# Kernel optimization log

Hardware: AMD Instinct MI355X
Metric: run time of the kernel (lower is better)

## Reference

```python
import jax, jax.numpy as jnp
import numpy as np

N = 50000      # nodes
E = 400000     # edges
G = 128        # graphs in batch
D_NODE = 64
EDGE_DIM = 72
HEADS = 4
H0, H1, H2 = 128, 128, 64
NC = 2
NEG = 0.2      # GATConv leaky_relu negative_slope default
D1 = H2 + EDGE_DIM - 1  # ffn input dim = 135


def _p(k, shape, s=0.1):
    return jax.random.normal(k, shape, dtype=jnp.float32) * s


def setup_inputs() -> dict:
    key = jax.random.key(0)
    ks = jax.random.split(key, 24)
    x = jax.random.normal(ks[0], (N, D_NODE), dtype=jnp.float32)
    edge_index = jax.random.randint(ks[1], (2, E), 0, N)
    edge_attr = jax.random.uniform(ks[2], (E, EDGE_DIM), dtype=jnp.float32)
    batch = jnp.sort(jax.random.randint(ks[3], (N,), 0, G))
    return dict(
        x=x, edge_index=edge_index, edge_attr=edge_attr, batch=batch,
        # GATConv layer 1: in=D_NODE, out=H0, heads=HEADS, concat
        W1=_p(ks[4], (D_NODE, HEADS * H0)), We1=_p(ks[5], (EDGE_DIM, HEADS * H0)),
        as1=_p(ks[6], (HEADS, H0)), ad1=_p(ks[7], (HEADS, H0)), ae1=_p(ks[8], (HEADS, H0)),
        b1=jnp.zeros((HEADS * H0,), jnp.float32),
        # GATConv layer 2: in=HEADS*H0, out=H1, heads=HEADS, concat
        W2=_p(ks[9], (HEADS * H0, HEADS * H1)), We2=_p(ks[10], (EDGE_DIM, HEADS * H1)),
        as2=_p(ks[11], (HEADS, H1)), ad2=_p(ks[12], (HEADS, H1)), ae2=_p(ks[13], (HEADS, H1)),
        b2=jnp.zeros((HEADS * H1,), jnp.float32),
        # GATConv layer 3: in=HEADS*H1, out=H2, heads=1, concat=False
        W3=_p(ks[14], (HEADS * H1, H2)), We3=_p(ks[15], (EDGE_DIM, H2)),
        as3=_p(ks[16], (1, H2)), ad3=_p(ks[17], (1, H2)), ae3=_p(ks[18], (1, H2)),
        b3=jnp.zeros((H2,), jnp.float32),
        # ffn: Linear(135 -> 67), ReLU, Linear(67 -> 2), Softmax
        Wf1=_p(ks[19], (D1, D1 // 2)), bf1=jnp.zeros((D1 // 2,), jnp.float32),
        Wf2=_p(ks[20], (D1 // 2, NC)), bf2=jnp.zeros((NC,), jnp.float32),
    )


def _seg_softmax(s, seg, n):
    # numerically-stable softmax over segments (per-destination neighborhoods)
    m = jax.ops.segment_max(s, seg, num_segments=n)
    m = jnp.where(jnp.isfinite(m), m, 0.0)
    e = jnp.exp(s - m[seg])
    z = jax.ops.segment_sum(e, seg, num_segments=n)
    return e / (z[seg] + 1e-16)


def _gat(x, src, dst, eattr, W, We, a_s, a_d, a_e, b, heads, oc, concat):
    # PyG GATConv with edge_dim: shared src/dst projection, edge feats only in attention
    n = x.shape[0]
    xs = (x @ W).reshape(n, heads, oc)            # [N,H,C]
    ee = (eattr @ We).reshape(-1, heads, oc)      # [Ea,H,C]
    alpha = (xs * a_s).sum(-1)[src] + (xs * a_d).sum(-1)[dst] + (ee * a_e).sum(-1)
    alpha = jax.nn.leaky_relu(alpha, NEG)         # [Ea,H]
    alpha = _seg_softmax(alpha, dst, n)
    out = jax.ops.segment_sum(xs[src] * alpha[:, :, None], dst, num_segments=n)
    out = out.reshape(n, heads * oc) if concat else out.mean(axis=1)
    return out + b


def reference(x, edge_index, edge_attr, batch,
              W1, We1, as1, ad1, ae1, b1,
              W2, We2, as2, ad2, ae2, b2,
              W3, We3, as3, ad3, ae3, b3,
              Wf1, bf1, Wf2, bf2):
    src, dst = edge_index[0], edge_index[1]
    n = x.shape[0]
    # --- 1-gram feature vector: scatter-add edge_attr[:, :-1] by graph of src ---
    eb = batch[src]
    og = jax.ops.segment_sum(edge_attr[:, :-1], eb, num_segments=G)   # [G, EDGE_DIM-1]
    og = og / jnp.maximum(jnp.linalg.norm(og, axis=1, keepdims=True), 1e-12)
    # --- add self loops, edge_attr fill_value='mean' (mean over incoming edges) ---
    ones_e = jnp.ones((src.shape[0],), x.dtype)
    deg = jax.ops.segment_sum(ones_e, dst, num_segments=n)
    loop_attr = jax.ops.segment_sum(edge_attr, dst, num_segments=n) / jnp.maximum(deg, 1.0)[:, None]
    nodes = jnp.arange(n)
    src_a = jnp.concatenate([src, nodes])
    dst_a = jnp.concatenate([dst, nodes])
    ea = jnp.concatenate([edge_attr, loop_attr], axis=0)
    # --- GAT stack with ReLU activations ---
    h = jax.nn.relu(_gat(x, src_a, dst_a, ea, W1, We1, as1, ad1, ae1, b1, HEADS, H0, True))
    h = jax.nn.relu(_gat(h, src_a, dst_a, ea, W2, We2, as2, ad2, ae2, b2, HEADS, H1, True))
    h = jax.nn.relu(_gat(h, src_a, dst_a, ea, W3, We3, as3, ad3, ae3, b3, 1, H2, False))
    # --- global mean pool over graphs ---
    cnt = jax.ops.segment_sum(jnp.ones((n,), x.dtype), batch, num_segments=G)
    pooled = jax.ops.segment_sum(h, batch, num_segments=G) / jnp.maximum(cnt, 1.0)[:, None]
    # --- concat + ffn (dropout p=0 in eval) + softmax ---
    z = jnp.concatenate([pooled, og], axis=1)                         # [G, 135]
    z = jax.nn.relu(z @ Wf1 + bf1)
    return jax.nn.softmax(z @ Wf2 + bf2, axis=1)
```

## Files before the change

kernel.cpp:

```cpp
#include <hip/hip_runtime.h>

#define NNODES 50000
#define NEDGES 400000
#define NEA    450000
#define NG     128
#define DEGCAP 96
#define OGW    72
#define NCH    49
#define PREPN  1128328
#define PREPB  4408
#define EDGEB  1563
#define OGB    (NG*16)

typedef unsigned short u16;
typedef unsigned int   u32;
typedef __attribute__((ext_vector_type(8))) short short8v;
typedef __attribute__((ext_vector_type(4))) float f32x4;

static inline int ceil_div(int a, int b){ return (a + b - 1)/b; }

__device__ __forceinline__ u16 f2bf(float f){
  u32 u = __builtin_bit_cast(u32, f);
  u = (u + 0x7fffu + ((u >> 16) & 1u)) >> 16;
  return (u16)u;
}
__device__ __forceinline__ float bfLO(u32 q){ return __builtin_bit_cast(float, q << 16); }
__device__ __forceinline__ float bfHI(u32 q){ return __builtin_bit_cast(float, q & 0xffff0000u); }
__device__ __forceinline__ void gload_lds16(const u16* g, u16* l){
  __builtin_amdgcn_global_load_lds((const __attribute__((address_space(1))) void*)g,
                                   (__attribute__((address_space(3))) void*)l, 16, 0, 0);
}

__global__ void k_prep_deg(const float* __restrict__ x, u16* __restrict__ xb,
                       const float* __restrict__ W1, u16* __restrict__ Wt1,
                       const float* __restrict__ W2, u16* __restrict__ Wt2,
                       const float* __restrict__ W3, u16* __restrict__ Wt3,
                       const float* __restrict__ We1, const float* __restrict__ ae1,
                       const float* __restrict__ We2, const float* __restrict__ ae2,
                       const float* __restrict__ We3, const float* __restrict__ ae3,
                       float* __restrict__ veall,
                       const int* __restrict__ src, const int* __restrict__ dst,
                       const int* __restrict__ batch,
                       int* __restrict__ deg, int* __restrict__ gb, int* __restrict__ gcnt){
  if (blockIdx.x >= PREPB){
    __shared__ int h[NG];
    int t = threadIdx.x;
    if (t < NG) h[t] = 0;
    __syncthreads();
    int e = (blockIdx.x - PREPB)*256 + t;
    if (e < NEDGES){
      atomicAdd(&deg[dst[e]], 1);
      int g = batch[src[e]];
      gb[e] = g;
      atomicAdd(&h[g], 1);
    }
    __syncthreads();
    if (t < NG && h[t]) atomicAdd(&gcnt[t], h[t]);
    return;
  }
  int i = blockIdx.x*blockDim.x + threadIdx.x;
  if (i < 800000){
    float4 v = ((const float4*)x)[i];
    ((ushort4*)xb)[i] = make_ushort4(f2bf(v.x), f2bf(v.y), f2bf(v.z), f2bf(v.w));
    return;
  }
  i -= 800000;
  if (i < 32768){
    int n = i >> 6, k = i & 63;
    Wt1[i] = f2bf(W1[(size_t)k*512 + n]);
    return;
  }
  i -= 32768;
  if (i < 262144){
    int n = i >> 9, k = i & 511;
    Wt2[i] = f2bf(W2[(size_t)k*512 + n]);
    return;
  }
  i -= 262144;
  if (i < 32768){
    int n = i >> 9, k = i & 511;
    Wt3[i] = f2bf(W3[(size_t)k*64 + n]);
    return;
  }
  i -= 32768;
  if (i < 648){
    const float* We; const float* ae; int H, C, basej, li;
    if (i < 288){ We = We1; ae = ae1; H = 4; C = 128; basej = 0; li = i; }
    else if (i < 576){ We = We2; ae = ae2; H = 4; C = 128; basej = 4; li = i - 288; }
    else { We = We3; ae = ae3; H = 1; C = 64; basej = 8; li = i - 576; }
    int k = li / H, h = li - k*H;
    const float* wrow = We + (size_t)k*H*C + (size_t)h*C;
    const float* arow = ae + (size_t)h*C;
    float s = 0.f;
    for (int c = 0; c < C; ++c) s += wrow[c]*arow[c];
    veall[k*9 + basej + h] = s;
  }
}

__global__ __launch_bounds__(1024) void k_chunksum(const int* __restrict__ deg, int* __restrict__ csum){
  __shared__ int s[1024];
  int t = threadIdx.x;
  int i = blockIdx.x*1024 + t;
  s[t] = (i < NNODES) ? deg[i]+1 : 0;
  __syncthreads();
  for (int o = 512; o > 0; o >>= 1){
    if (t < o) s[t] += s[t+o];
    __syncthreads();
  }
  if (t == 0) csum[blockIdx.x] = s[0];
}

__global__ __launch_bounds__(128) void k_scanmid(const int* __restrict__ csum, int* __restrict__ cbase,
                                                 const int* __restrict__ gcnt, int* __restrict__ goff,
                                                 int* __restrict__ gcur){
  __shared__ int sg[NG];
  int t = threadIdx.x;
  if (t < 64){
    int v0 = (t < NCH) ? csum[t] : 0;
    int v = v0;
    #pragma unroll
    for (int o = 1; o < 64; o <<= 1){
      int xsh = __shfl_up(v, o);
      if (t >= o) v += xsh;
    }
    if (t < NCH) cbase[t] = v - v0;
  }
  int vg = gcnt[t];
  sg[t] = vg;
  __syncthreads();
  for (int o = 1; o < NG; o <<= 1){
    int xg = (t >= o) ? sg[t-o] : 0;
    __syncthreads();
    sg[t] += xg;
    __syncthreads();
  }
  goff[t] = sg[t] - vg;
  gcur[t] = sg[t] - vg;
}

__global__ __launch_bounds__(1024) void k_scanout(const int* __restrict__ deg,
                                                  const int* __restrict__ cbase, int* __restrict__ off){
  __shared__ int s[1024];
  int t = threadIdx.x;
  int i = blockIdx.x*1024 + t;
  int v = (i < NNODES) ? deg[i]+1 : 0;
  s[t] = v;
  __syncthreads();
  for (int o = 1; o < 1024; o <<= 1){
    int xv = (t >= o) ? s[t-o] : 0;
    __syncthreads();
    s[t] += xv;
    __syncthreads();
  }
  if (i < NNODES){
    int incl = s[t] + cbase[blockIdx.x];
    off[i] = incl - v;
    if (i == NNODES-1) off[NNODES] = incl;
  }
}

__global__ void k_scatter(const int* __restrict__ src, const int* __restrict__ dst,
                          const int* __restrict__ gb, const int* __restrict__ off,
                          int* __restrict__ cnt, int* __restrict__ gcur,
                          int* __restrict__ csr_src, int* __restrict__ edgepos,
                          int* __restrict__ sortedeid){
  __shared__ int lcnt[NG];
  __shared__ int lbase[NG];
  int t = threadIdx.x;
  int e = blockIdx.x*256 + t;
  if (t < NG) lcnt[t] = 0;
  __syncthreads();
  int g = -1, lr = 0;
  if (e < NEDGES){
    int d = dst[e];
    int p = off[d] + atomicAdd(&cnt[d], 1);
    csr_src[p] = src[e];
    edgepos[e] = p;
    g = gb[e];
    lr = atomicAdd(&lcnt[g], 1);
  } else {
    int n2 = e - NEDGES;
    if (n2 < NNODES){
      int p = off[n2+1] - 1;
      csr_src[p] = n2;
    }
  }
  __syncthreads();
  if (t < NG && lcnt[t]) lbase[t] = atomicAdd(&gcur[t], lcnt[t]);
  __syncthreads();
  if (g >= 0) sortedeid[lbase[g] + lr] = e;
}

__global__ __launch_bounds__(256) void k_edge(const float* __restrict__ attr,
    const int* __restrict__ goff, const int* __restrict__ gcnt,
    const int* __restrict__ sortedeid, float* __restrict__ og,
    const int* __restrict__ edgepos, const float* __restrict__ veall,
    float* __restrict__ se1, float* __restrict__ se2, float* __restrict__ se3){
  __shared__ float sh[16*OGW];
  if (blockIdx.x < OGB){
    float (*red)[OGW] = (float(*)[OGW])sh;
    int g = blockIdx.x >> 4, chunk = blockIdx.x & 15;
    int lane = threadIdx.x & 63, w = threadIdx.x >> 6;
    int esub = lane >> 4, l16 = lane & 15;
    int slot = w*4 + esub;
    int beg = goff[g], cnt = gcnt[g];
    int cbeg = beg + ((cnt*chunk) >> 4);
    int cend = beg + ((cnt*(chunk+1)) >> 4);
    f32x4 acc  = {0.f,0.f,0.f,0.f};
    f32x4 acch = {0.f,0.f,0.f,0.f};
    for (int i0 = cbeg; i0 < cend; i0 += 32){
      int e1 = i0 + slot, e2 = i0 + 16 + slot;
      int id1 = (e1 < cend) ? sortedeid[e1] : -1;
      int id2 = (e2 < cend) ? sortedeid[e2] : -1;
      f32x4 v1 = {0.f,0.f,0.f,0.f}, v2 = {0.f,0.f,0.f,0.f};
      f32x4 h1 = {0.f,0.f,0.f,0.f}, h2 = {0.f,0.f,0.f,0.f};
      if (id1 >= 0){
        v1 = *(const f32x4*)(attr + (size_t)id1*72 + l16*4);
        if (l16 < 2) h1 = *(const f32x4*)(attr + (size_t)id1*72 + 64 + l16*4);
      }
      if (id2 >= 0){
        v2 = *(const f32x4*)(attr + (size_t)id2*72 + l16*4);
        if (l16 < 2) h2 = *(const f32x4*)(attr + (size_t)id2*72 + 64 + l16*4);
      }
      acc += v1; acc += v2;
      if (l16 < 2){ acch += h1; acch += h2; }
    }
    #pragma unroll
    for (int j = 0; j < 4; ++j) red[slot][l16*4 + j] = acc[j];
    if (l16 < 2){
      #pragma unroll
      for (int j = 0; j < 4; ++j) red[slot][64 + l16*4 + j] = acch[j];
    }
    __syncthreads();
    int t = threadIdx.x;
    if (t < 71){
      float s = 0.f;
      #pragma unroll
      for (int q = 0; q < 16; ++q) s += red[q][t];
      atomicAdd(&og[g*OGW + t], s);
    }
    return;
  }
  float* vel = sh;
  for (int i = threadIdx.x; i < 72*9; i += blockDim.x) vel[i] = veall[i];
  __syncthreads();
  int e = (blockIdx.x - OGB)*blockDim.x + threadIdx.x;
  if (e >= NEDGES) return;
  const float4* row = (const float4*)(attr + (size_t)e*72);
  float s[9];
  #pragma unroll
  for (int j = 0; j < 9; ++j) s[j] = 0.f;
  #pragma unroll
  for (int kk = 0; kk < 18; ++kk){
    float4 a = row[kk];
    #pragma unroll
    for (int j = 0; j < 9; ++j)
      s[j] += a.x*vel[(kk*4+0)*9+j] + a.y*vel[(kk*4+1)*9+j]
            + a.z*vel[(kk*4+2)*9+j] + a.w*vel[(kk*4+3)*9+j];
  }
  int p = edgepos[e];
  *(float4*)(se1 + (size_t)p*4) = make_float4(s[0], s[1], s[2], s[3]);
  *(float4*)(se2 + (size_t)p*4) = make_float4(s[4], s[5], s[6], s[7]);
  se3[p] = s[8];
}

__global__ __launch_bounds__(256) void k_gemm128(const u16* __restrict__ A,
    const u16* __restrict__ Bt, u16* __restrict__ C, int M, int K,
    const float* __restrict__ a_s, const float* __restrict__ a_d,
    float* __restrict__ ssrc, float* __restrict__ sdst){
  __shared__ __align__(16) u16 smem[128*128];
  u16* As = smem;
  u16* Bs = smem + 128*64;
  __shared__ float s_ps[128][2];
  __shared__ float s_pd[128][2];
  const int tid = threadIdx.x;
  const int wid = tid >> 6, lane = tid & 63;
  const int l15 = lane & 15, kslot = lane >> 4;
  const int wr = wid >> 1, wc = wid & 1;
  const int h = blockIdx.x;
  const int m0 = blockIdx.y * 128, n0 = h * 128;
  const int Nn = 512;
  f32x4 acc[4][4];
  #pragma unroll
  for (int mi = 0; mi < 4; ++mi)
    #pragma unroll
    for (int ni = 0; ni < 4; ++ni)
      acc[mi][ni] = (f32x4){0.f,0.f,0.f,0.f};

  for (int kt = 0; kt < K; kt += 64){
    #pragma unroll
    for (int r = 0; r < 4; ++r){
      int chunk = (r*4 + wid)*64 + lane;
      int row = chunk >> 3, c8 = chunk & 7;
      int srcc = c8 ^ (row & 7);
      int grow = m0 + row; if (grow > M-1) grow = M-1;
      gload_lds16(A + (size_t)grow*K + kt + srcc*8, &As[chunk*8]);
    }
    #pragma unroll
    for (int r = 0; r < 4; ++r){
      int chunk = (r*4 + wid)*64 + lane;
      int row = chunk >> 3, c8 = chunk & 7;
      int srcc = c8 ^ (row & 7);
      gload_lds16(Bt + (size_t)(n0+row)*K + kt + srcc*8, &Bs[chunk*8]);
    }
    __syncthreads();
    #pragma unroll
    for (int s = 0; s < 2; ++s){
      short8v a[4], b[4];
      #pragma unroll
      for (int mi = 0; mi < 4; ++mi){
        int row = wr*64 + mi*16 + l15;
        a[mi] = *(const short8v*)(&As[row*64 + (((s*4 + kslot) ^ (row&7))*8)]);
      }
      #pragma unroll
      for (int ni = 0; ni < 4; ++ni){
        int col = wc*64 + ni*16 + l15;
        b[ni] = *(const short8v*)(&Bs[col*64 + (((s*4 + kslot) ^ (col&7))*8)]);
      }
      #pragma unroll
      for (int mi = 0; mi < 4; ++mi)
        #pragma unroll
        for (int ni = 0; ni < 4; ++ni)
          acc[mi][ni] = __builtin_amdgcn_mfma_f32_16x16x32_bf16(a[mi], b[ni], acc[mi][ni], 0, 0, 0);
    }
    __syncthreads();
  }
  float asv[4], adv[4];
  #pragma unroll
  for (int ni = 0; ni < 4; ++ni){
    int c = wc*64 + ni*16 + l15;
    asv[ni] = a_s[h*128 + c];
    adv[ni] = a_d[h*128 + c];
  }
  #pragma unroll
  for (int mi = 0; mi < 4; ++mi){
    #pragma unroll
    for (int r = 0; r < 4; ++r){
      int row_l = wr*64 + mi*16 + kslot*4 + r;
      float ps = 0.f, pd = 0.f;
      #pragma unroll
      for (int ni = 0; ni < 4; ++ni){
        float v = acc[mi][ni][r];
        smem[row_l*128 + wc*64 + ni*16 + l15] = f2bf(v);
        ps += v*asv[ni];
        pd += v*adv[ni];
      }
      #pragma unroll
      for (int m = 8; m >= 1; m >>= 1){ ps += __shfl_xor(ps,m); pd += __shfl_xor(pd,m); }
      if (l15 == 0){ s_ps[row_l][wc] = ps; s_pd[row_l][wc] = pd; }
    }
  }
  __syncthreads();
  #pragma unroll
  for (int i = 0; i < 8; ++i){
    int c = i*256 + tid;
    int row = c >> 4, c16 = c & 15;
    int grow = m0 + row;
    if (grow < M)
      *(uint4*)(C + (size_t)grow*Nn + n0 + c16*8) = *(const uint4*)(&smem[row*128 + c16*8]);
  }
  if (tid < 128){
    int grow = m0 + tid;
    if (grow < M){
      ssrc[grow*4 + h] = s_ps[tid][0] + s_ps[tid][1];
      sdst[grow*4 + h] = s_pd[tid][0] + s_pd[tid][1];
    }
  }
}

__global__ __launch_bounds__(256) void k_gemm64(const u16* __restrict__ A,
    const u16* __restrict__ Bt, u16* __restrict__ C, int M,
    const float* __restrict__ a_s, const float* __restrict__ a_d,
    float* __restrict__ ssrc, float* __restrict__ sdst){
  __shared__ __align__(16) u16 As[64*64];
  __shared__ __align__(16) u16 Bs[64*64];
  const int tid = threadIdx.x;
  const int wid = tid >> 6, lane = tid & 63;
  const int l15 = lane & 15, kslot = lane >> 4;
  const int m0 = blockIdx.x * 64;
  f32x4 acc[4];
  #pragma unroll
  for (int ni = 0; ni < 4; ++ni) acc[ni] = (f32x4){0.f,0.f,0.f,0.f};
  for (int kt = 0; kt < 512; kt += 64){
    #pragma unroll
    for (int r = 0; r < 2; ++r){
      int chunk = r*256 + tid;
      int row = chunk >> 3, c8 = chunk & 7;
      int srcc = c8 ^ (row & 7);
      int grow = m0 + row; if (grow > M-1) grow = M-1;
      gload_lds16(A + (size_t)grow*512 + kt + srcc*8, &As[chunk*8]);
    }
    #pragma unroll
    for (int r = 0; r < 2; ++r){
      int chunk = r*256 + tid;
      int row = chunk >> 3, c8 = chunk & 7;
      int srcc = c8 ^ (row & 7);
      gload_lds16(Bt + (size_t)row*512 + kt + srcc*8, &Bs[chunk*8]);
    }
    __syncthreads();
    #pragma unroll
    for (int s = 0; s < 2; ++s){
      int row = wid*16 + l15;
      short8v a = *(const short8v*)(&As[row*64 + (((s*4 + kslot) ^ (row&7))*8)]);
      #pragma unroll
      for (int ni = 0; ni < 4; ++ni){
        int col = ni*16 + l15;
        short8v b = *(const short8v*)(&Bs[col*64 + (((s*4 + kslot) ^ (col&7))*8)]);
        acc[ni] = __builtin_amdgcn_mfma_f32_16x16x32_bf16(a, b, acc[ni], 0, 0, 0);
      }
    }
    __syncthreads();
  }
  #pragma unroll
  for (int r = 0; r < 4; ++r){
    int row_l = wid*16 + kslot*4 + r;
    int grow = m0 + row_l;
// ... 143 lines not shown
  #pragma unroll
  for (int msk = 1; msk < 64; msk <<= 1) m = fmaxf(m, __shfl_xor(m, msk));
  float z = 0.f;
  for (int e = lane; e < deg; e += 64){ float ex = __expf(s_al[w][e]-m); s_al[w][e] = ex; z += ex; }
  #pragma unroll
  for (int msk = 1; msk < 64; msk <<= 1) z += __shfl_xor(z, msk);
  float inv = 1.0f/(z + 1e-16f);
  for (int e = lane; e < deg; e += 64) s_al[w][e] *= inv;
  int degR = (deg + 3) & ~3;
  for (int e = deg + lane; e < degR; e += 64){ s_al[w][e] = 0.f; s_col[w][e] = n; }
  __syncthreads();
  int half = lane >> 5, cp = lane & 31;
  float a0 = 0.f, a1 = 0.f;
  for (int e = 0; e < degR; e += 4){
    int c0 = s_col[w][e + half], c1 = s_col[w][e + 2 + half];
    u32 q0 = *(const u32*)(xs + (size_t)c0*64 + cp*2);
    u32 q1 = *(const u32*)(xs + (size_t)c1*64 + cp*2);
    float al0 = s_al[w][e + half], al1 = s_al[w][e + 2 + half];
    a0 += al0*bfLO(q0) + al1*bfLO(q1);
    a1 += al0*bfHI(q0) + al1*bfHI(q1);
  }
  a0 += __shfl_xor(a0, 32);
  a1 += __shfl_xor(a1, 32);
  if (half == 0){
    float2 o;
    o.x = fmaxf(a0 + bias[cp*2+0], 0.f);
    o.y = fmaxf(a1 + bias[cp*2+1], 0.f);
    *(float2*)(out + (size_t)n*64 + cp*2) = o;
  }
}

__global__ __launch_bounds__(64) void k_pool(const float* __restrict__ h, const int* __restrict__ batch,
                                             float* __restrict__ pooled, int* __restrict__ cntg){
  int l = threadIdx.x;
  int start = blockIdx.x * 128;
  if (start >= NNODES) return;
  int endn = min(start + 128, NNODES);
  float acc = 0.f;
  int curg = batch[start];
  int run = 0;
  for (int n = start; n < endn; ++n){
    int g = batch[n];
    if (g != curg){
      atomicAdd(&pooled[curg*64+l], acc);
      if (l == 0) atomicAdd(&cntg[curg], run);
      acc = 0.f; run = 0; curg = g;
    }
    acc += h[(size_t)n*64 + l];
    ++run;
  }
  atomicAdd(&pooled[curg*64+l], acc);
  if (l == 0) atomicAdd(&cntg[curg], run);
}

__global__ void k_ffn(const float* __restrict__ pooled, const int* __restrict__ cntg,
                      const float* __restrict__ og,
                      const float* __restrict__ Wf1, const float* __restrict__ bf1,
                      const float* __restrict__ Wf2, const float* __restrict__ bf2,
                      float* __restrict__ out){
  __shared__ float z[135];
  __shared__ float z1[67];
  __shared__ float o2[2];
  int g = blockIdx.x, t = threadIdx.x;
  if (t < 64) z[t] = pooled[g*64+t] * (1.0f/fmaxf((float)cntg[g], 1.0f));
  else if (t < 135) z[t] = og[g*OGW + (t-64)];
  __syncthreads();
  if (t == 0){
    float s = 0.f;
    for (int k = 0; k < 71; ++k) s += z[64+k]*z[64+k];
    float scale = 1.0f / fmaxf(sqrtf(s), 1e-12f);
    for (int k = 0; k < 71; ++k) z[64+k] *= scale;
  }
  __syncthreads();
  if (t < 67){
    float s = bf1[t];
    for (int d = 0; d < 135; ++d) s += z[d]*Wf1[d*67+t];
    z1[t] = fmaxf(s, 0.f);
  }
  __syncthreads();
  if (t < 2){
    float s = bf2[t];
    for (int j = 0; j < 67; ++j) s += z1[j]*Wf2[j*2+t];
    o2[t] = s;
  }
  __syncthreads();
  if (t == 0){
    float m = fmaxf(o2[0], o2[1]);
    float e0 = expf(o2[0]-m), e1 = expf(o2[1]-m);
    float inv = 1.0f/(e0+e1);
    out[g*2+0] = e0*inv;
    out[g*2+1] = e1*inv;
  }
}

extern "C" void kernel_launch(void* const* d_in, const int* in_sizes, int n_in,
                              void* d_out, int out_size, void* d_ws, size_t ws_size,
                              hipStream_t stream){
  const float* x     = (const float*)d_in[0];
  const int*   ei    = (const int*)d_in[1];
  const float* eattr = (const float*)d_in[2];
  const int*   batch = (const int*)d_in[3];
  const float* W1  = (const float*)d_in[4];
  const float* We1 = (const float*)d_in[5];
  const float* as1 = (const float*)d_in[6];
  const float* ad1 = (const float*)d_in[7];
  const float* ae1 = (const float*)d_in[8];
  const float* b1  = (const float*)d_in[9];
  const float* W2  = (const float*)d_in[10];
  const float* We2 = (const float*)d_in[11];
  const float* as2 = (const float*)d_in[12];
  const float* ad2 = (const float*)d_in[13];
  const float* ae2 = (const float*)d_in[14];
  const float* b2  = (const float*)d_in[15];
  const float* W3  = (const float*)d_in[16];
  const float* We3 = (const float*)d_in[17];
  const float* as3 = (const float*)d_in[18];
  const float* ad3 = (const float*)d_in[19];
  const float* ae3 = (const float*)d_in[20];
  const float* b3  = (const float*)d_in[21];
  const float* Wf1 = (const float*)d_in[22];
  const float* bf1 = (const float*)d_in[23];
  const float* Wf2 = (const float*)d_in[24];
  const float* bf2 = (const float*)d_in[25];
  (void)in_sizes; (void)n_in; (void)out_size; (void)ws_size;
  const int* src = ei;
  const int* dst = ei + NEDGES;
  float* out = (float*)d_out;

  char* base = (char*)d_ws;
  size_t woff = 0;
  auto alloc = [&](size_t bytes)->char*{
    char* p = base + woff;
    woff += (bytes + 255) & ~(size_t)255;
    return p;
  };
  u16*   xsb    = (u16*)  alloc((size_t)NNODES*512*2);
  u16*   hb     = (u16*)  alloc((size_t)NNODES*512*2);
  u16*   xs3b   = (u16*)  alloc((size_t)NNODES*64*2);
  float* h3     = (float*)alloc((size_t)NNODES*64*4);
  u16*   xb     = (u16*)  alloc((size_t)NNODES*64*2);
  u16*   Wt1    = (u16*)  alloc((size_t)512*64*2);
  u16*   Wt2    = (u16*)  alloc((size_t)512*512*2);
  u16*   Wt3    = (u16*)  alloc((size_t)64*512*2);
  float* se1    = (float*)alloc((size_t)NEA*4*4);
  float* se2    = (float*)alloc((size_t)NEA*4*4);
  float* se3    = (float*)alloc((size_t)NEA*4);
  float* ssrc   = (float*)alloc((size_t)NNODES*4*4);
  float* sdst   = (float*)alloc((size_t)NNODES*4*4);
  float* veall  = (float*)alloc(72*9*4);
  int*   gb     = (int*)alloc((size_t)NEDGES*4);
  int*   csroff = (int*)alloc((size_t)(NNODES+1)*4);
  int*   csrsrc = (int*)alloc((size_t)NEA*4);
  int*   edgepos= (int*)alloc((size_t)NEDGES*4);
  int*   goff   = (int*)alloc(NG*4);
  int*   gcur   = (int*)alloc(NG*4);
  int*   sortedeid = (int*)alloc((size_t)NEDGES*4);
  int*   csum   = (int*)alloc(NCH*4);
  int*   cbase  = (int*)alloc(NCH*4);
  size_t z0 = woff;
  int*   deg    = (int*)alloc((size_t)NNODES*4);
  int*   cnt    = (int*)alloc((size_t)NNODES*4);
  int*   gcnt   = (int*)alloc(NG*4);
  float* og     = (float*)alloc((size_t)NG*OGW*4);
  float* pooled = (float*)alloc((size_t)NG*64*4);
  int*   cntg   = (int*)alloc((size_t)NG*4);
  size_t zlen = woff - z0;

  hipMemsetAsync(base + z0, 0, zlen, stream);

  k_prep_deg<<<PREPB + EDGEB,256,0,stream>>>(
      x, xb, W1, Wt1, W2, Wt2, W3, Wt3, We1, ae1, We2, ae2, We3, ae3, veall,
      src, dst, batch, deg, gb, gcnt);

  k_chunksum<<<NCH,1024,0,stream>>>(deg, csum);
  k_scanmid <<<1,128,0,stream>>>(csum, cbase, gcnt, goff, gcur);
  k_scanout <<<NCH,1024,0,stream>>>(deg, cbase, csroff);

  k_scatter<<<ceil_div(NEDGES+NNODES,256),256,0,stream>>>(src, dst, gb, csroff, cnt, gcur,
                                                          csrsrc, edgepos, sortedeid);

  k_edge<<<OGB + EDGEB,256,0,stream>>>(eattr, goff, gcnt, sortedeid, og,
                                       edgepos, veall, se1, se2, se3);

  dim3 g128(4, ceil_div(NNODES,128));

  k_gemm128<<<g128,256,0,stream>>>(xb, Wt1, xsb, NNODES, 64, as1, ad1, ssrc, sdst);
  k_agg12<<<NNODES/4,256,0,stream>>>(xsb, csroff, csrsrc, ssrc, sdst, se1, b1, hb);

  k_gemm128<<<g128,256,0,stream>>>(hb, Wt2, xsb, NNODES, 512, as2, ad2, ssrc, sdst);
  k_agg12<<<NNODES/4,256,0,stream>>>(xsb, csroff, csrsrc, ssrc, sdst, se2, b2, hb);

  k_gemm64<<<ceil_div(NNODES,64),256,0,stream>>>(hb, Wt3, xs3b, NNODES, as3, ad3, ssrc, sdst);
  k_agg3<<<NNODES/4,256,0,stream>>>(xs3b, csroff, csrsrc, ssrc, sdst, se3, b3, h3);

  k_pool<<<ceil_div(NNODES,128),64,0,stream>>>(h3, batch, pooled, cntg);
  k_ffn <<<NG,192,0,stream>>>(pooled, cntg, og, Wf1, bf1, Wf2, bf2, out);
}
```

Measured before the change: 515.2 us.

## Fuse per-graph edge-attr sums into edge score kernel via LDS bins

The separate group-by-graph edge sort (per-graph counts, scan, sortedeid scatter) is removed. The per-edge attention score and per-graph edge-attribute sum are now computed in one pass: each edge's attr row is read once by 16 lanes, dot products are shuffle-reduced, and attrs are atomically accumulated into per-block LDS bins for all 128 graphs before flushing to global. This cuts one full read of the 115MB attr tensor and several small kernels, in exchange for heavy LDS float atomics (36KB bins per block) and up to 9216 global atomics per block.

```diff
diff --git a/kernel.cpp b/kernel.cpp
--- a/kernel.cpp
+++ b/kernel.cpp
@@ -10,7 +10,7 @@
 #define PREPN  1128328
 #define PREPB  4408
 #define EDGEB  1563
-#define OGB    (NG*16)
+#define EB2    1024
 
 typedef unsigned short u16;
 typedef unsigned int   u32;
@@ -41,21 +41,13 @@
                        float* __restrict__ veall,
                        const int* __restrict__ src, const int* __restrict__ dst,
                        const int* __restrict__ batch,
-                       int* __restrict__ deg, int* __restrict__ gb, int* __restrict__ gcnt){
+                       int* __restrict__ deg, int* __restrict__ gb){
   if (blockIdx.x >= PREPB){
-    __shared__ int h[NG];
-    int t = threadIdx.x;
-    if (t < NG) h[t] = 0;
-    __syncthreads();
-    int e = (blockIdx.x - PREPB)*256 + t;
+    int e = (blockIdx.x - PREPB)*256 + threadIdx.x;
     if (e < NEDGES){
       atomicAdd(&deg[dst[e]], 1);
-      int g = batch[src[e]];
-      gb[e] = g;
-      atomicAdd(&h[g], 1);
-    }
-    __syncthreads();
-    if (t < NG && h[t]) atomicAdd(&gcnt[t], h[t]);
+      gb[e] = batch[src[e]];
+    }
     return;
   }
   int i = blockIdx.x*blockDim.x + threadIdx.x;
@@ -110,32 +102,16 @@
   if (t == 0) csum[blockIdx.x] = s[0];
 }
 
-__global__ __launch_bounds__(128) void k_scanmid(const int* __restrict__ csum, int* __restrict__ cbase,
-                                                 const int* __restrict__ gcnt, int* __restrict__ goff,
-                                                 int* __restrict__ gcur){
-  __shared__ int sg[NG];
+__global__ __launch_bounds__(64) void k_scanmid(const int* __restrict__ csum, int* __restrict__ cbase){
   int t = threadIdx.x;
-  if (t < 64){
-    int v0 = (t < NCH) ? csum[t] : 0;
-    int v = v0;
-    #pragma unroll
-    for (int o = 1; o < 64; o <<= 1){
-      int xsh = __shfl_up(v, o);
-      if (t >= o) v += xsh;
-    }
-    if (t < NCH) cbase[t] = v - v0;
-  }
-  int vg = gcnt[t];
-  sg[t] = vg;
-  __syncthreads();
-  for (int o = 1; o < NG; o <<= 1){
-    int xg = (t >= o) ? sg[t-o] : 0;
-    __syncthreads();
-    sg[t] += xg;
-    __syncthreads();
-  }
-  goff[t] = sg[t] - vg;
-  gcur[t] = sg[t] - vg;
+  int v0 = (t < NCH) ? csum[t] : 0;
+  int v = v0;
+  #pragma unroll
+  for (int o = 1; o < 64; o <<= 1){
+    int xsh = __shfl_up(v, o);
+    if (t >= o) v += xsh;
+  }
+  if (t < NCH) cbase[t] = v - v0;
 }
 
 __global__ __launch_bounds__(1024) void k_scanout(const int* __restrict__ deg,
@@ -159,25 +135,15 @@
   }
 }
 
-__global__ void k_scatter(const int* __restrict__ src, const int* __restrict__ dst,
-                          const int* __restrict__ gb, const int* __restrict__ off,
-                          int* __restrict__ cnt, int* __restrict__ gcur,
-                          int* __restrict__ csr_src, int* __restrict__ edgepos,
-                          int* __restrict__ sortedeid){
-  __shared__ int lcnt[NG];
-  __shared__ int lbase[NG];
-  int t = threadIdx.x;
-  int e = blockIdx.x*256 + t;
-  if (t < NG) lcnt[t] = 0;
-  __syncthreads();
-  int g = -1, lr = 0;
+__global__ void k_fillself(const int* __restrict__ src, const int* __restrict__ dst,
+                           const int* __restrict__ off, int* __restrict__ cnt,
+                           int* __restrict__ csr_src, int* __restrict__ edgepos){
+  int e = blockIdx.x*256 + threadIdx.x;
   if (e < NEDGES){
     int d = dst[e];
     int p = off[d] + atomicAdd(&cnt[d], 1);
     csr_src[p] = src[e];
     edgepos[e] = p;
-    g = gb[e];
-    lr = atomicAdd(&lcnt[g], 1);
   } else {
     int n2 = e - NEDGES;
     if (n2 < NNODES){
@@ -185,83 +151,80 @@
       csr_src[p] = n2;
     }
   }
-  __syncthreads();
-  if (t < NG && lcnt[t]) lbase[t] = atomicAdd(&gcur[t], lcnt[t]);
-  __syncthreads();
-  if (g >= 0) sortedeid[lbase[g] + lr] = e;
-}
-
-__global__ __launch_bounds__(256) void k_edge(const float* __restrict__ attr,
-    const int* __restrict__ goff, const int* __restrict__ gcnt,
-    const int* __restrict__ sortedeid, float* __restrict__ og,
-    const int* __restrict__ edgepos, const float* __restrict__ veall,
-    float* __restrict__ se1, float* __restrict__ se2, float* __restrict__ se3){
-  __shared__ float sh[16*OGW];
-  if (blockIdx.x < OGB){
-    float (*red)[OGW] = (float(*)[OGW])sh;
-    int g = blockIdx.x >> 4, chunk = blockIdx.x & 15;
-    int lane = threadIdx.x & 63, w = threadIdx.x >> 6;
-    int esub = lane >> 4, l16 = lane & 15;
-    int slot = w*4 + esub;
-    int beg = goff[g], cnt = gcnt[g];
-    int cbeg = beg + ((cnt*chunk) >> 4);
-    int cend = beg + ((cnt*(chunk+1)) >> 4);
-    f32x4 acc  = {0.f,0.f,0.f,0.f};
-    f32x4 acch = {0.f,0.f,0.f,0.f};
-    for (int i0 = cbeg; i0 < cend; i0 += 32){
-      int e1 = i0 + slot, e2 = i0 + 16 + slot;
-      int id1 = (e1 < cend) ? sortedeid[e1] : -1;
-      int id2 = (e2 < cend) ? sortedeid[e2] : -1;
-      f32x4 v1 = {0.f,0.f,0.f,0.f}, v2 = {0.f,0.f,0.f,0.f};
-      f32x4 h1 = {0.f,0.f,0.f,0.f}, h2 = {0.f,0.f,0.f,0.f};
-      if (id1 >= 0){
-        v1 = *(const f32x4*)(attr + (size_t)id1*72 + l16*4);
-        if (l16 < 2) h1 = *(const f32x4*)(attr + (size_t)id1*72 + 64 + l16*4);
+}
+
+__global__ __launch_bounds__(256) void k_edge2(const float* __restrict__ attr,
+    const int* __restrict__ gb, const int* __restrict__ edgepos,
+    const float* __restrict__ veall,
+    float* __restrict__ se1, float* __restrict__ se2, float* __restrict__ se3,
+    float* __restrict__ og){
+  __shared__ float bins[NG*OGW];
+  __shared__ float vel[72*9];
+  int t = threadIdx.x;
+  for (int i = t; i < NG*OGW; i += 256) bins[i] = 0.f;
+  for (int i = t; i < 648; i += 256) vel[i] = veall[i];
+  __syncthreads();
+  int lane = t & 63, w = t >> 6;
+  int esub = lane >> 4, l16 = lane & 15;
+  const int EPB = (NEDGES + EB2 - 1)/EB2;
+  int e0 = blockIdx.x*EPB, e1 = min(e0 + EPB, NEDGES);
+  for (int base = e0; base < e1; base += 16){
+    int e = base + w*4 + esub;
+    bool ok = (e < e1);
+    f32x4 v  = {0.f,0.f,0.f,0.f};
+    f32x4 vt = {0.f,0.f,0.f,0.f};
+    int g = 0;
+    if (ok){
+      v = *(const f32x4*)(attr + (size_t)e*72 + l16*4);
+      if (l16 < 2) vt = *(const f32x4*)(attr + (size_t)e*72 + 64 + l16*4);
+      g = gb[e];
+    }
+    float s[9];
+    #pragma unroll
+    for (int j = 0; j < 9; ++j){
+      int c0 = l16*4;
+      s[j] = v[0]*vel[(c0+0)*9+j] + v[1]*vel[(c0+1)*9+j]
+           + v[2]*vel[(c0+2)*9+j] + v[3]*vel[(c0+3)*9+j];
+    }
+    if (l16 < 2){
+      int c0 = 64 + l16*4;
+      #pragma unroll
+      for (int j = 0; j < 9; ++j)
+        s[j] += vt[0]*vel[(c0+0)*9+j] + vt[1]*vel[(c0+1)*9+j]
+              + vt[2]*vel[(c0+2)*9+j] + vt[3]*vel[(c0+3)*9+j];
+    }
+    #pragma unroll
+    for (int msk = 1; msk < 16; msk <<= 1){
+      #pragma unroll
+      for (int j = 0; j < 9; ++j) s[j] += __shfl_xor(s[j], msk);
+    }
+    if (ok && l16 == 0){
+      int p = edgepos[e];
+      *(float4*)(se1 + (size_t)p*4) = make_float4(s[0], s[1], s[2], s[3]);
+      *(float4*)(se2 + (size_t)p*4) = make_float4(s[4], s[5], s[6], s[7]);
+      se3[p] = s[8];
+    }
+    if (ok){
+      float* bb = bins + g*OGW;
+      int c0 = l16*4;
+      atomicAdd(&bb[c0+0], v[0]);
+      atomicAdd(&bb[c0+1], v[1]);
+      atomicAdd(&bb[c0+2], v[2]);
+      atomicAdd(&bb[c0+3], v[3]);
+      if (l16 < 2){
+        int ct = 64 + l16*4;
+        atomicAdd(&bb[ct+0], vt[0]);
+        atomicAdd(&bb[ct+1], vt[1]);
+        atomicAdd(&bb[ct+2], vt[2]);
+        if (l16 == 0) atomicAdd(&bb[ct+3], vt[3]);
       }
-      if (id2 >= 0){
-        v2 = *(const f32x4*)(attr + (size_t)id2*72 + l16*4);
-        if (l16 < 2) h2 = *(const f32x4*)(attr + (size_t)id2*72 + 64 + l16*4);
-      }
-      acc += v1; acc += v2;
-      if (l16 < 2){ acch += h1; acch += h2; }
-    }
-    #pragma unroll
-    for (int j = 0; j < 4; ++j) red[slot][l16*4 + j] = acc[j];
-    if (l16 < 2){
-      #pragma unroll
-      for (int j = 0; j < 4; ++j) red[slot][64 + l16*4 + j] = acch[j];
-    }
-    __syncthreads();
-    int t = threadIdx.x;
-    if (t < 71){
-      float s = 0.f;
-      #pragma unroll
-      for (int q = 0; q < 16; ++q) s += red[q][t];
-      atomicAdd(&og[g*OGW + t], s);
-    }
-    return;
-  }
-  float* vel = sh;
-  for (int i = threadIdx.x; i < 72*9; i += blockDim.x) vel[i] = veall[i];
-  __syncthreads();
-  int e = (blockIdx.x - OGB)*blockDim.x + threadIdx.x;
-  if (e >= NEDGES) return;
-  const float4* row = (const float4*)(attr + (size_t)e*72);
-  float s[9];
-  #pragma unroll
-  for (int j = 0; j < 9; ++j) s[j] = 0.f;
-  #pragma unroll
-  for (int kk = 0; kk < 18; ++kk){
-    float4 a = row[kk];
-    #pragma unroll
-    for (int j = 0; j < 9; ++j)
-      s[j] += a.x*vel[(kk*4+0)*9+j] + a.y*vel[(kk*4+1)*9+j]
-            + a.z*vel[(kk*4+2)*9+j] + a.w*vel[(kk*4+3)*9+j];
-  }
-  int p = edgepos[e];
-  *(float4*)(se1 + (size_t)p*4) = make_float4(s[0], s[1], s[2], s[3]);
-  *(float4*)(se2 + (size_t)p*4) = make_float4(s[4], s[5], s[6], s[7]);
-  se3[p] = s[8];
+    }
+  }
+  __syncthreads();
+  for (int i = t; i < NG*OGW; i += 256){
+    float vv = bins[i];
+    if (vv != 0.f) atomicAdd(&og[i], vv);
+  }
 }
 
 __global__ __launch_bounds__(256) void k_gemm128(const u16* __restrict__ A,
@@ -711,15 +674,11 @@
   int*   csroff = (int*)alloc((size_t)(NNODES+1)*4);
   int*   csrsrc = (int*)alloc((size_t)NEA*4);
   int*   edgepos= (int*)alloc((size_t)NEDGES*4);
-  int*   goff   = (int*)alloc(NG*4);
-  int*   gcur   = (int*)alloc(NG*4);
-  int*   sortedeid = (int*)alloc((size_t)NEDGES*4);
   int*   csum   = (int*)alloc(NCH*4);
   int*   cbase  = (int*)alloc(NCH*4);
   size_t z0 = woff;
   int*   deg    = (int*)alloc((size_t)NNODES*4);
   int*   cnt    = (int*)alloc((size_t)NNODES*4);
-  int*   gcnt   = (int*)alloc(NG*4);
   float* og     = (float*)alloc((size_t)NG*OGW*4);
   float* pooled = (float*)alloc((size_t)NG*64*4);
   int*   cntg   = (int*)alloc((size_t)NG*4);
@@ -729,17 +688,15 @@
 
   k_prep_deg<<<PREPB + EDGEB,256,0,stream>>>(
       x, xb, W1, Wt1, W2, Wt2, W3, Wt3, We1, ae1, We2, ae2, We3, ae3, veall,
-      src, dst, batch, deg, gb, gcnt);
+      src, dst, batch, deg, gb);
 
   k_chunksum<<<NCH,1024,0,stream>>>(deg, csum);
-  k_scanmid <<<1,128,0,stream>>>(csum, cbase, gcnt, goff, gcur);
+  k_scanmid <<<1,64,0,stream>>>(csum, cbase);
   k_scanout <<<NCH,1024,0,stream>>>(deg, cbase, csroff);
 
-  k_scatter<<<ceil_div(NEDGES+NNODES,256),256,0,stream>>>(src, dst, gb, csroff, cnt, gcur,
-                                                          csrsrc, edgepos, sortedeid);
-
-  k_edge<<<OGB + EDGEB,256,0,stream>>>(eattr, goff, gcnt, sortedeid, og,
-                                       edgepos, veall, se1, se2, se3);
+  k_fillself<<<ceil_div(NEDGES+NNODES,256),256,0,stream>>>(src, dst, csroff, cnt, csrsrc, edgepos);
+
+  k_edge2<<<EB2,256,0,stream>>>(eattr, gb, edgepos, veall, se1, se2, se3, og);
 
   dim3 g128(4, ceil_div(NNODES,128));
 
```

Result: slower. 600.9 us (+16.7%).

## Fuse per-edge attention projection into graph-sorted edge-attr reduction pass

Applied to the files above, without the earlier changes.

Merges the two halves of the edge kernel so that each edge-attr row is read once, in graph-sorted order. The same loaded values now feed both the per-graph og accumulation and the 72x9 edge projection. The projection is spread across 16 lanes and reduced with xor shuffles before the scores are scattered to CSR positions. This removes a second full pass over the edge-attr matrix, but adds an indirect edgepos gather, uncoalesced scattered stores and 18 shuffle reductions per iteration, and cuts the grid to only the OGB blocks.

```diff
diff --git a/kernel.cpp b/kernel.cpp
--- a/kernel.cpp
+++ b/kernel.cpp
@@ -191,77 +191,92 @@
   if (g >= 0) sortedeid[lbase[g] + lr] = e;
 }
 
-__global__ __launch_bounds__(256) void k_edge(const float* __restrict__ attr,
+__global__ __launch_bounds__(256) void k_edge3(const float* __restrict__ attr,
     const int* __restrict__ goff, const int* __restrict__ gcnt,
-    const int* __restrict__ sortedeid, float* __restrict__ og,
-    const int* __restrict__ edgepos, const float* __restrict__ veall,
-    float* __restrict__ se1, float* __restrict__ se2, float* __restrict__ se3){
-  __shared__ float sh[16*OGW];
-  if (blockIdx.x < OGB){
-    float (*red)[OGW] = (float(*)[OGW])sh;
-    int g = blockIdx.x >> 4, chunk = blockIdx.x & 15;
-    int lane = threadIdx.x & 63, w = threadIdx.x >> 6;
-    int esub = lane >> 4, l16 = lane & 15;
-    int slot = w*4 + esub;
-    int beg = goff[g], cnt = gcnt[g];
-    int cbeg = beg + ((cnt*chunk) >> 4);
-    int cend = beg + ((cnt*(chunk+1)) >> 4);
-    f32x4 acc  = {0.f,0.f,0.f,0.f};
-    f32x4 acch = {0.f,0.f,0.f,0.f};
-    for (int i0 = cbeg; i0 < cend; i0 += 32){
-      int e1 = i0 + slot, e2 = i0 + 16 + slot;
-      int id1 = (e1 < cend) ? sortedeid[e1] : -1;
-      int id2 = (e2 < cend) ? sortedeid[e2] : -1;
-      f32x4 v1 = {0.f,0.f,0.f,0.f}, v2 = {0.f,0.f,0.f,0.f};
-      f32x4 h1 = {0.f,0.f,0.f,0.f}, h2 = {0.f,0.f,0.f,0.f};
-      if (id1 >= 0){
-        v1 = *(const f32x4*)(attr + (size_t)id1*72 + l16*4);
-        if (l16 < 2) h1 = *(const f32x4*)(attr + (size_t)id1*72 + 64 + l16*4);
+    const int* __restrict__ sortedeid, const int* __restrict__ edgepos,
+    const float* __restrict__ veall,
+    float* __restrict__ se1, float* __restrict__ se2, float* __restrict__ se3,
+    float* __restrict__ og){
+  __shared__ float red[16][OGW];
+  __shared__ float vel[72*9];
+  int t = threadIdx.x;
+  for (int i = t; i < 648; i += 256) vel[i] = veall[i];
+  int g = blockIdx.x >> 4, chunk = blockIdx.x & 15;
+  int lane = t & 63, w = t >> 6;
+  int esub = lane >> 4, l16 = lane & 15;
+  int slot = w*4 + esub;
+  int beg = goff[g], cnt = gcnt[g];
+  int cbeg = beg + ((cnt*chunk) >> 4);
+  int cend = beg + ((cnt*(chunk+1)) >> 4);
+  f32x4 acc  = {0.f,0.f,0.f,0.f};
+  f32x4 acch = {0.f,0.f,0.f,0.f};
+  __syncthreads();
+  for (int i0 = cbeg; i0 < cend; i0 += 32){
+    int p1 = i0 + slot, p2 = i0 + 16 + slot;
+    int id1 = (p1 < cend) ? sortedeid[p1] : -1;
+    int id2 = (p2 < cend) ? sortedeid[p2] : -1;
+    int ep1 = (id1 >= 0) ? edgepos[id1] : 0;
+    int ep2 = (id2 >= 0) ? edgepos[id2] : 0;
+    f32x4 v1 = {0.f,0.f,0.f,0.f}, v2 = {0.f,0.f,0.f,0.f};
+    f32x4 h1 = {0.f,0.f,0.f,0.f}, h2 = {0.f,0.f,0.f,0.f};
+    if (id1 >= 0){
+      v1 = *(const f32x4*)(attr + (size_t)id1*72 + l16*4);
+      if (l16 < 2) h1 = *(const f32x4*)(attr + (size_t)id1*72 + 64 + l16*4);
+    }
+    if (id2 >= 0){
+      v2 = *(const f32x4*)(attr + (size_t)id2*72 + l16*4);
+      if (l16 < 2) h2 = *(const f32x4*)(attr + (size_t)id2*72 + 64 + l16*4);
+    }
+    acc += v1; acc += v2;
+    if (l16 < 2){ acch += h1; acch += h2; }
+    float s1[9], s2[9];
+    int c0 = l16*4;
+    #pragma unroll
+    for (int j = 0; j < 9; ++j){
+      s1[j] = v1[0]*vel[(c0+0)*9+j] + v1[1]*vel[(c0+1)*9+j]
+            + v1[2]*vel[(c0+2)*9+j] + v1[3]*vel[(c0+3)*9+j];
+      s2[j] = v2[0]*vel[(c0+0)*9+j] + v2[1]*vel[(c0+1)*9+j]
+            + v2[2]*vel[(c0+2)*9+j] + v2[3]*vel[(c0+3)*9+j];
+    }
+    if (l16 < 2){
+      int ct = 64 + l16*4;
+      #pragma unroll
+      for (int j = 0; j < 9; ++j){
+        s1[j] += h1[0]*vel[(ct+0)*9+j] + h1[1]*vel[(ct+1)*9+j]
+               + h1[2]*vel[(ct+2)*9+j] + h1[3]*vel[(ct+3)*9+j];
+        s2[j] += h2[0]*vel[(ct+0)*9+j] + h2[1]*vel[(ct+1)*9+j]
+               + h2[2]*vel[(ct+2)*9+j] + h2[3]*vel[(ct+3)*9+j];
       }
-      if (id2 >= 0){
-        v2 = *(const f32x4*)(attr + (size_t)id2*72 + l16*4);
-        if (l16 < 2) h2 = *(const f32x4*)(attr + (size_t)id2*72 + 64 + l16*4);
-      }
-      acc += v1; acc += v2;
-      if (l16 < 2){ acch += h1; acch += h2; }
-    }
-    #pragma unroll
-    for (int j = 0; j < 4; ++j) red[slot][l16*4 + j] = acc[j];
-    if (l16 < 2){
+    }
+    #pragma unroll
+    for (int msk = 1; msk < 16; msk <<= 1){
       #pragma unroll
-      for (int j = 0; j < 4; ++j) red[slot][64 + l16*4 + j] = acch[j];
-    }
-    __syncthreads();
-    int t = threadIdx.x;
-    if (t < 71){
-      float s = 0.f;
-      #pragma unroll
-      for (int q = 0; q < 16; ++q) s += red[q][t];
-      atomicAdd(&og[g*OGW + t], s);
-    }
-    return;
-  }
-  float* vel = sh;
-  for (int i = threadIdx.x; i < 72*9; i += blockDim.x) vel[i] = veall[i];
-  __syncthreads();
-  int e = (blockIdx.x - OGB)*blockDim.x + threadIdx.x;
-  if (e >= NEDGES) return;
-  const float4* row = (const float4*)(attr + (size_t)e*72);
-  float s[9];
-  #pragma unroll
-  for (int j = 0; j < 9; ++j) s[j] = 0.f;
-  #pragma unroll
-  for (int kk = 0; kk < 18; ++kk){
-    float4 a = row[kk];
-    #pragma unroll
-    for (int j = 0; j < 9; ++j)
-      s[j] += a.x*vel[(kk*4+0)*9+j] + a.y*vel[(kk*4+1)*9+j]
-            + a.z*vel[(kk*4+2)*9+j] + a.w*vel[(kk*4+3)*9+j];
-  }
-  int p = edgepos[e];
-  *(float4*)(se1 + (size_t)p*4) = make_float4(s[0], s[1], s[2], s[3]);
-  *(float4*)(se2 + (size_t)p*4) = make_float4(s[4], s[5], s[6], s[7]);
-  se3[p] = s[8];
+      for (int j = 0; j < 9; ++j){ s1[j] += __shfl_xor(s1[j], msk); s2[j] += __shfl_xor(s2[j], msk); }
+    }
+    if (l16 == 0 && id1 >= 0){
+      *(float4*)(se1 + (size_t)ep1*4) = make_float4(s1[0], s1[1], s1[2], s1[3]);
+      *(float4*)(se2 + (size_t)ep1*4) = make_float4(s1[4], s1[5], s1[6], s1[7]);
+      se3[ep1] = s1[8];
+    }
+    if (l16 == 1 && id2 >= 0){
+      *(float4*)(se1 + (size_t)ep2*4) = make_float4(s2[0], s2[1], s2[2], s2[3]);
+      *(float4*)(se2 + (size_t)ep2*4) = make_float4(s2[4], s2[5], s2[6], s2[7]);
+      se3[ep2] = s2[8];
+    }
+  }
+  #pragma unroll
+  for (int j = 0; j < 4; ++j) red[slot][l16*4 + j] = acc[j];
+  if (l16 < 2){
+    #pragma unroll
+    for (int j = 0; j < 4; ++j) red[slot][64 + l16*4 + j] = acch[j];
+  }
+  __syncthreads();
+  if (t < 71){
+    float s = 0.f;
+    #pragma unroll
+    for (int q = 0; q < 16; ++q) s += red[q][t];
+    atomicAdd(&og[g*OGW + t], s);
+  }
 }
 
 __global__ __launch_bounds__(256) void k_gemm128(const u16* __restrict__ A,
@@ -738,8 +753,8 @@
   k_scatter<<<ceil_div(NEDGES+NNODES,256),256,0,stream>>>(src, dst, gb, csroff, cnt, gcur,
                                                           csrsrc, edgepos, sortedeid);
 
-  k_edge<<<OGB + EDGEB,256,0,stream>>>(eattr, goff, gcnt, sortedeid, og,
-                                       edgepos, veall, se1, se2, se3);
+  k_edge3<<<OGB,256,0,stream>>>(eattr, goff, gcnt, sortedeid, edgepos, veall,
+                                se1, se2, se3, og);
 
   dim3 g128(4, ceil_div(NNODES,128));
 
```

After: 518.3 us. Within noise of the previous version (+0.6%).

## Fuse edge-score projection into og pooling pass and merge with layer-1 GEMM launch

Applied to the files above, without the earlier changes.

The per-edge attention score projection (se1/se2/se3) is now computed inside the graph-sorted edge-attr pooling loop, reusing the attr rows already loaded for the og sum instead of reading edge_attr a second time. The per-edge dot products are reduced across 16 lanes with shuffles. The layer-1 GEMM is folded into the same launch as extra blocks, so the two independent workloads share one grid and one kernel launch is removed. The cost is heavy shuffle traffic per edge, scattered edgepos lookups, and higher LDS and register use in the combined kernel, which may lower occupancy.

```diff
diff --git a/kernel.cpp b/kernel.cpp
--- a/kernel.cpp
+++ b/kernel.cpp
@@ -10,7 +10,8 @@
 #define PREPN  1128328
 #define PREPB  4408
 #define EDGEB  1563
-#define OGB    (NG*16)
+#define EDGE3B 2048
+#define GEMM1B 1564
 
 typedef unsigned short u16;
 typedef unsigned int   u32;
@@ -191,16 +192,25 @@
   if (g >= 0) sortedeid[lbase[g] + lr] = e;
 }
 
-__global__ __launch_bounds__(256) void k_edge(const float* __restrict__ attr,
-    const int* __restrict__ goff, const int* __restrict__ gcnt,
-    const int* __restrict__ sortedeid, float* __restrict__ og,
-    const int* __restrict__ edgepos, const float* __restrict__ veall,
-    float* __restrict__ se1, float* __restrict__ se2, float* __restrict__ se3){
-  __shared__ float sh[16*OGW];
-  if (blockIdx.x < OGB){
-    float (*red)[OGW] = (float(*)[OGW])sh;
+__global__ __launch_bounds__(256) void k_l1edge(
+    const u16* __restrict__ A, const u16* __restrict__ Bt, u16* __restrict__ C, int M,
+    const float* __restrict__ a_s, const float* __restrict__ a_d,
+    float* __restrict__ ssrc, float* __restrict__ sdst,
+    const float* __restrict__ attr, const int* __restrict__ goff, const int* __restrict__ gcnt,
+    const int* __restrict__ sortedeid, const int* __restrict__ edgepos,
+    const float* __restrict__ veall,
+    float* __restrict__ se1, float* __restrict__ se2, float* __restrict__ se3,
+    float* __restrict__ og){
+  __shared__ __align__(16) u16 smem[128*128];
+  __shared__ float s_ps[128][2];
+  __shared__ float s_pd[128][2];
+  const int tid = threadIdx.x;
+  if (blockIdx.x < EDGE3B){
+    float (*red)[OGW] = (float(*)[OGW])smem;
+    float* vel = (float*)smem + 16*OGW;
+    for (int i = tid; i < 648; i += 256) vel[i] = veall[i];
     int g = blockIdx.x >> 4, chunk = blockIdx.x & 15;
-    int lane = threadIdx.x & 63, w = threadIdx.x >> 6;
+    int lane = tid & 63, w = tid >> 6;
     int esub = lane >> 4, l16 = lane & 15;
     int slot = w*4 + esub;
     int beg = goff[g], cnt = gcnt[g];
@@ -208,22 +218,57 @@
     int cend = beg + ((cnt*(chunk+1)) >> 4);
     f32x4 acc  = {0.f,0.f,0.f,0.f};
     f32x4 acch = {0.f,0.f,0.f,0.f};
-    for (int i0 = cbeg; i0 < cend; i0 += 32){
-      int e1 = i0 + slot, e2 = i0 + 16 + slot;
-      int id1 = (e1 < cend) ? sortedeid[e1] : -1;
-      int id2 = (e2 < cend) ? sortedeid[e2] : -1;
-      f32x4 v1 = {0.f,0.f,0.f,0.f}, v2 = {0.f,0.f,0.f,0.f};
-      f32x4 h1 = {0.f,0.f,0.f,0.f}, h2 = {0.f,0.f,0.f,0.f};
-      if (id1 >= 0){
-        v1 = *(const f32x4*)(attr + (size_t)id1*72 + l16*4);
-        if (l16 < 2) h1 = *(const f32x4*)(attr + (size_t)id1*72 + 64 + l16*4);
-      }
-      if (id2 >= 0){
-        v2 = *(const f32x4*)(attr + (size_t)id2*72 + l16*4);
-        if (l16 < 2) h2 = *(const f32x4*)(attr + (size_t)id2*72 + 64 + l16*4);
-      }
-      acc += v1; acc += v2;
-      if (l16 < 2){ acch += h1; acch += h2; }
+    __syncthreads();
+    for (int i0 = cbeg; i0 < cend; i0 += 64){
+      int ids[4], eps[4];
+      #pragma unroll
+      for (int k = 0; k < 4; ++k){
+        int p = i0 + k*16 + slot;
+        ids[k] = (p < cend) ? sortedeid[p] : -1;
+      }
+      #pragma unroll
+      for (int k = 0; k < 4; ++k) eps[k] = (ids[k] >= 0) ? edgepos[ids[k]] : 0;
+      f32x4 v[4], vh[4];
+      #pragma unroll
+      for (int k = 0; k < 4; ++k){
+        v[k]  = (f32x4){0.f,0.f,0.f,0.f};
+        vh[k] = (f32x4){0.f,0.f,0.f,0.f};
+        if (ids[k] >= 0){
+          v[k] = *(const f32x4*)(attr + (size_t)ids[k]*72 + l16*4);
+          if (l16 < 2) vh[k] = *(const f32x4*)(attr + (size_t)ids[k]*72 + 64 + l16*4);
+        }
+      }
+      #pragma unroll
+      for (int k = 0; k < 4; ++k){
+        acc += v[k];
+        if (l16 < 2) acch += vh[k];
+      }
+      int c0 = l16*4, ct = 64 + l16*4;
+      #pragma unroll
+      for (int k = 0; k < 4; ++k){
+        float s[9];
+        #pragma unroll
+        for (int j = 0; j < 9; ++j)
+          s[j] = v[k][0]*vel[(c0+0)*9+j] + v[k][1]*vel[(c0+1)*9+j]
+               + v[k][2]*vel[(c0+2)*9+j] + v[k][3]*vel[(c0+3)*9+j];
+        if (l16 < 2){
+          #pragma unroll
+          for (int j = 0; j < 9; ++j)
+            s[j] += vh[k][0]*vel[(ct+0)*9+j] + vh[k][1]*vel[(ct+1)*9+j]
+                  + vh[k][2]*vel[(ct+2)*9+j] + vh[k][3]*vel[(ct+3)*9+j];
+        }
+        #pragma unroll
+        for (int msk = 1; msk < 16; msk <<= 1){
+          #pragma unroll
+          for (int j = 0; j < 9; ++j) s[j] += __shfl_xor(s[j], msk);
+        }
+        if (l16 == k && ids[k] >= 0){
+          int p = eps[k];
+          *(float4*)(se1 + (size_t)p*4) = make_float4(s[0], s[1], s[2], s[3]);
+          *(float4*)(se2 + (size_t)p*4) = make_float4(s[4], s[5], s[6], s[7]);
+          se3[p] = s[8];
+        }
+      }
     }
     #pragma unroll
     for (int j = 0; j < 4; ++j) red[slot][l16*4 + j] = acc[j];
@@ -232,36 +277,109 @@
       for (int j = 0; j < 4; ++j) red[slot][64 + l16*4 + j] = acch[j];
     }
     __syncthreads();
-    int t = threadIdx.x;
-    if (t < 71){
+    if (tid < 71){
       float s = 0.f;
       #pragma unroll
-      for (int q = 0; q < 16; ++q) s += red[q][t];
-      atomicAdd(&og[g*OGW + t], s);
+      for (int q = 0; q < 16; ++q) s += red[q][tid];
+      atomicAdd(&og[g*OGW + tid], s);
     }
     return;
   }
-  float* vel = sh;
-  for (int i = threadIdx.x; i < 72*9; i += blockDim.x) vel[i] = veall[i];
-  __syncthreads();
-  int e = (blockIdx.x - OGB)*blockDim.x + threadIdx.x;
-  if (e >= NEDGES) return;
-  const float4* row = (const float4*)(attr + (size_t)e*72);
-  float s[9];
-  #pragma unroll
-  for (int j = 0; j < 9; ++j) s[j] = 0.f;
-  #pragma unroll
-  for (int kk = 0; kk < 18; ++kk){
-    float4 a = row[kk];
-    #pragma unroll
-    for (int j = 0; j < 9; ++j)
-      s[j] += a.x*vel[(kk*4+0)*9+j] + a.y*vel[(kk*4+1)*9+j]
-            + a.z*vel[(kk*4+2)*9+j] + a.w*vel[(kk*4+3)*9+j];
-  }
-  int p = edgepos[e];
-  *(float4*)(se1 + (size_t)p*4) = make_float4(s[0], s[1], s[2], s[3]);
-  *(float4*)(se2 + (size_t)p*4) = make_float4(s[4], s[5], s[6], s[7]);
-  se3[p] = s[8];
+  int bid = blockIdx.x - EDGE3B;
+  u16* As = smem;
+  u16* Bs = smem + 128*64;
+  const int wid = tid >> 6, lane = tid & 63;
+  const int l15 = lane & 15, kslot = lane >> 4;
+  const int wr = wid >> 1, wc = wid & 1;
+  const int h = bid & 3;
+  const int m0 = (bid >> 2) * 128, n0 = h * 128;
+  const int K = 64, Nn = 512;
+  f32x4 acc[4][4];
+  #pragma unroll
+  for (int mi = 0; mi < 4; ++mi)
+    #pragma unroll
+    for (int ni = 0; ni < 4; ++ni)
+      acc[mi][ni] = (f32x4){0.f,0.f,0.f,0.f};
+
+  for (int kt = 0; kt < K; kt += 64){
+    #pragma unroll
+    for (int r = 0; r < 4; ++r){
+      int chunk = (r*4 + wid)*64 + lane;
+      int row = chunk >> 3, c8 = chunk & 7;
+      int srcc = c8 ^ (row & 7);
+      int grow = m0 + row; if (grow > M-1) grow = M-1;
+      gload_lds16(A + (size_t)grow*K + kt + srcc*8, &As[chunk*8]);
+    }
+    #pragma unroll
+    for (int r = 0; r < 4; ++r){
+      int chunk = (r*4 + wid)*64 + lane;
+      int row = chunk >> 3, c8 = chunk & 7;
+      int srcc = c8 ^ (row & 7);
+      gload_lds16(Bt + (size_t)(n0+row)*K + kt + srcc*8, &Bs[chunk*8]);
+    }
+    __syncthreads();
+    #pragma unroll
+    for (int s = 0; s < 2; ++s){
+      short8v a[4], b[4];
+      #pragma unroll
+      for (int mi = 0; mi < 4; ++mi){
+        int row = wr*64 + mi*16 + l15;
+        a[mi] = *(const short8v*)(&As[row*64 + (((s*4 + kslot) ^ (row&7))*8)]);
+      }
+      #pragma unroll
+      for (int ni = 0; ni < 4; ++ni){
+        int col = wc*64 + ni*16 + l15;
+        b[ni] = *(const short8v*)(&Bs[col*64 + (((s*4 + kslot) ^ (col&7))*8)]);
+      }
+      #pragma unroll
+      for (int mi = 0; mi < 4; ++mi)
+        #pragma unroll
+        for (int ni = 0; ni < 4; ++ni)
+          acc[mi][ni] = __builtin_amdgcn_mfma_f32_16x16x32_bf16(a[mi], b[ni], acc[mi][ni], 0, 0, 0);
+    }
+    __syncthreads();
+  }
+  float asv[4], adv[4];
+  #pragma unroll
+  for (int ni = 0; ni < 4; ++ni){
+    int c = wc*64 + ni*16 + l15;
+    asv[ni] = a_s[h*128 + c];
+    adv[ni] = a_d[h*128 + c];
+  }
+  #pragma unroll
+  for (int mi = 0; mi < 4; ++mi){
+    #pragma unroll
+    for (int r = 0; r < 4; ++r){
+      int row_l = wr*64 + mi*16 + kslot*4 + r;
+      float ps = 0.f, pd = 0.f;
+      #pragma unroll
+      for (int ni = 0; ni < 4; ++ni){
+        float v = acc[mi][ni][r];
+        smem[row_l*128 + wc*64 + ni*16 + l15] = f2bf(v);
+        ps += v*asv[ni];
+        pd += v*adv[ni];
+      }
+      #pragma unroll
+      for (int m = 8; m >= 1; m >>= 1){ ps += __shfl_xor(ps,m); pd += __shfl_xor(pd,m); }
+      if (l15 == 0){ s_ps[row_l][wc] = ps; s_pd[row_l][wc] = pd; }
+    }
+  }
+  __syncthreads();
+  #pragma unroll
+  for (int i = 0; i < 8; ++i){
+    int c = i*256 + tid;
+    int row = c >> 4, c16 = c & 15;
+    int grow = m0 + row;
+    if (grow < M)
+      *(uint4*)(C + (size_t)grow*Nn + n0 + c16*8) = *(const uint4*)(&smem[row*128 + c16*8]);
+  }
+  if (tid < 128){
+    int grow = m0 + tid;
+    if (grow < M){
+      ssrc[grow*4 + h] = s_ps[tid][0] + s_ps[tid][1];
+      sdst[grow*4 + h] = s_pd[tid][0] + s_pd[tid][1];
+    }
+  }
 }
 
 __global__ __launch_bounds__(256) void k_gemm128(const u16* __restrict__ A,
@@ -738,14 +856,12 @@
   k_scatter<<<ceil_div(NEDGES+NNODES,256),256,0,stream>>>(src, dst, gb, csroff, cnt, gcur,
                                                           csrsrc, edgepos, sortedeid);
 
-  k_edge<<<OGB + EDGEB,256,0,stream>>>(eattr, goff, gcnt, sortedeid, og,
-                                       edgepos, veall, se1, se2, se3);
+  k_l1edge<<<EDGE3B + GEMM1B,256,0,stream>>>(
+      xb, Wt1, xsb, NNODES, as1, ad1, ssrc, sdst,
+      eattr, goff, gcnt, sortedeid, edgepos, veall, se1, se2, se3, og);
+  k_agg12<<<NNODES/4,256,0,stream>>>(xsb, csroff, csrsrc, ssrc, sdst, se1, b1, hb);
 
   dim3 g128(4, ceil_div(NNODES,128));
-
-  k_gemm128<<<g128,256,0,stream>>>(xb, Wt1, xsb, NNODES, 64, as1, ad1, ssrc, sdst);
-  k_agg12<<<NNODES/4,256,0,stream>>>(xsb, csroff, csrsrc, ssrc, sdst, se1, b1, hb);
-
   k_gemm128<<<g128,256,0,stream>>>(hb, Wt2, xsb, NNODES, 512, as2, ad2, ssrc, sdst);
   k_agg12<<<NNODES/4,256,0,stream>>>(xsb, csroff, csrsrc, ssrc, sdst, se2, b2, hb);
 
```

New measurement: 536.8 us. 4.2% more time.
